# Kernel optimization log

Measured on AMD Instinct MI355X. Metric: run time of the kernel, lower is better.

## Reference

```python
import jax, jax.numpy as jnp
import numpy as np

D_MODEL = 1024
NUM_HEADS = 16
D_K = D_MODEL // NUM_HEADS


def setup_inputs() -> dict:
    key = jax.random.key(0)
    ks = jax.random.split(key, 7)
    B, S = 4, 2048
    scale = 1.0 / np.sqrt(D_MODEL)
    return {
        "query": jax.random.normal(ks[0], (B, S, D_MODEL), dtype=jnp.float32),
        "key": jax.random.normal(ks[1], (B, S, D_MODEL), dtype=jnp.float32),
        "value": jax.random.normal(ks[2], (B, S, D_MODEL), dtype=jnp.float32),
        "W_q": jax.random.normal(ks[3], (D_MODEL, D_MODEL), dtype=jnp.float32) * scale,
        "W_k": jax.random.normal(ks[4], (D_MODEL, D_MODEL), dtype=jnp.float32) * scale,
        "W_v": jax.random.normal(ks[5], (D_MODEL, D_MODEL), dtype=jnp.float32) * scale,
        "W_o": jax.random.normal(ks[6], (D_MODEL, D_MODEL), dtype=jnp.float32) * scale,
    }


def reference(query, key, value, W_q, W_k, W_v, W_o):
    B, S, _ = query.shape
    # nn.Linear applies x @ W.T; project then split heads: (B, H, S, d_k)
    def proj(x, W):
        return (x @ W.T).reshape(B, S, NUM_HEADS, D_K).transpose(0, 2, 1, 3)
    Q = proj(query, W_q)
    K = proj(key, W_k)
    V = proj(value, W_v)
    # naive full-score attention: (B, H, S, S)
    scores = jnp.einsum("bhqd,bhkd->bhqk", Q, K) / jnp.sqrt(jnp.float32(D_K))
    attn = jax.nn.softmax(scores, axis=-1)
    out = jnp.einsum("bhqk,bhkd->bhqd", attn, V)  # (B, H, S, d_k)
    out = out.transpose(0, 2, 1, 3).reshape(B, S, D_MODEL)
    return out @ W_o.T
```

## Files before the change

kernel.cpp:

```cpp
#include <hip/hip_runtime.h>
#include <hip/hip_bf16.h>
#include <cstdint>
#include <cstddef>

static constexpr int S  = 2048;
static constexpr int DM = 1024;
static constexpr int NH = 16;
static constexpr int BB = 4;
static constexpr int MR = BB * S;

typedef __bf16 bf16x8 __attribute__((ext_vector_type(8)));
typedef float  f32x4  __attribute__((ext_vector_type(4)));
typedef float  f32x16 __attribute__((ext_vector_type(16)));
typedef unsigned int uint2v __attribute__((ext_vector_type(2)));

__device__ __forceinline__ f32x4 mfma16(bf16x8 a, bf16x8 b, f32x4 c) {
    return __builtin_amdgcn_mfma_f32_16x16x32_bf16(a, b, c, 0, 0, 0);
}
__device__ __forceinline__ f32x16 mfma32(bf16x8 a, bf16x8 b, f32x16 c) {
    return __builtin_amdgcn_mfma_f32_32x32x16_bf16(a, b, c, 0, 0, 0);
}

__device__ __forceinline__ unsigned int cvt_pk_bf16(float lo, float hi) {
    unsigned int r;
    asm("v_cvt_pk_bf16_f32 %0, %1, %2" : "=v"(r) : "v"(lo), "v"(hi));
    return r;
}

struct CvtArgs {
    const float* src[7];
    __hip_bfloat16* dst[7];
    int n[7];
    float scl[7];
};

__global__ __launch_bounds__(256) void cvt_kernel(CvtArgs a) {
    const int t = blockIdx.y;
    const int i = (blockIdx.x * 256 + threadIdx.x) * 4;
    if (i >= a.n[t]) return;
    const float s = a.scl[t];
    const float4 v = *reinterpret_cast<const float4*>(a.src[t] + i);
    union { __hip_bfloat16 h[4]; short4 s4; } u;
    u.h[0] = __float2bfloat16(v.x * s);
    u.h[1] = __float2bfloat16(v.y * s);
    u.h[2] = __float2bfloat16(v.z * s);
    u.h[3] = __float2bfloat16(v.w * s);
    *reinterpret_cast<short4*>(a.dst[t] + i) = u.s4;
}

template<int SPLIT>
__global__ __launch_bounds__(256) void gemm_bt(
    const __hip_bfloat16* __restrict__ X,
    const __hip_bfloat16* __restrict__ W,
    void* __restrict__ Cout, int M, int N, int K)
{
    __shared__ __align__(16) unsigned char smem[65536];
    __hip_bfloat16* Ts = reinterpret_cast<__hip_bfloat16*>(smem);

    const int tid  = threadIdx.x;
    const int wave = tid >> 6, lane = tid & 63;
    const int wm = wave >> 1, wn = wave & 1;
    const int lr = lane & 15, lg = lane >> 4;
    const int m0 = blockIdx.y * 128;
    const int n0 = blockIdx.x * 128;

    const int srow = tid >> 3, scol = (tid & 7) * 8;

    auto stage = [&](int bsel, int kt) {
        __hip_bfloat16* As = reinterpret_cast<__hip_bfloat16*>(smem + bsel * 32768);
        __hip_bfloat16* Bs = reinterpret_cast<__hip_bfloat16*>(smem + bsel * 32768 + 16384);
#pragma unroll
        for (int r = 0; r < 4; ++r) {
            const int c = r * 256 + tid;
            const int row = srow + r * 32;
            __builtin_amdgcn_global_load_lds(
                (const __attribute__((address_space(1))) void*)&X[(size_t)(m0 + row) * K + kt + scol],
                (__attribute__((address_space(3))) void*)&As[c * 8], 16, 0, 0);
            __builtin_amdgcn_global_load_lds(
                (const __attribute__((address_space(1))) void*)&W[(size_t)(n0 + row) * K + kt + scol],
                (__attribute__((address_space(3))) void*)&Bs[c * 8], 16, 0, 0);
        }
    };

    f32x4 acc[4][4] = {};

    stage(0, 0);
    int cur = 0;
    for (int kt = 0; kt < K; kt += 64) {
        __syncthreads();
        if (kt + 64 < K) stage(cur ^ 1, kt + 64);

        const __hip_bfloat16* As = reinterpret_cast<const __hip_bfloat16*>(smem + cur * 32768);
        const __hip_bfloat16* Bs = reinterpret_cast<const __hip_bfloat16*>(smem + cur * 32768 + 16384);
#pragma unroll
        for (int ks = 0; ks < 2; ++ks) {
            bf16x8 af[4], bfr[4];
#pragma unroll
            for (int i = 0; i < 4; ++i)
                af[i] = *reinterpret_cast<const bf16x8*>(&As[(wm * 64 + i * 16 + lr) * 64 + ks * 32 + lg * 8]);
#pragma unroll
            for (int i = 0; i < 4; ++i)
                bfr[i] = *reinterpret_cast<const bf16x8*>(&Bs[(wn * 64 + i * 16 + lr) * 64 + ks * 32 + lg * 8]);
#pragma unroll
            for (int mi = 0; mi < 4; ++mi)
#pragma unroll
                for (int ni = 0; ni < 4; ++ni)
                    acc[mi][ni] = mfma16(af[mi], bfr[ni], acc[mi][ni]);
        }
        cur ^= 1;
    }

    if constexpr (SPLIT == 2) {
        __syncthreads();
#pragma unroll
        for (int mi = 0; mi < 4; ++mi)
#pragma unroll
            for (int ni = 0; ni < 4; ++ni)
#pragma unroll
                for (int j = 0; j < 4; ++j) {
                    const int nl = wn * 64 + ni * 16 + lr;
                    const int ml = wm * 64 + mi * 16 + lg * 4 + j;
                    Ts[nl * 136 + ml] = __float2bfloat16(acc[mi][ni][j]);
                }
        __syncthreads();
        __hip_bfloat16* VT = reinterpret_cast<__hip_bfloat16*>(Cout);
        const int b = m0 >> 11, s0 = m0 & (S - 1);
#pragma unroll
        for (int r = 0; r < 8; ++r) {
            const int idx = r * 256 + tid;
            const int nl = idx >> 4, mc = idx & 15;
            const uint4 val = *reinterpret_cast<const uint4*>(&Ts[nl * 136 + mc * 8]);
            const int h = (n0 + nl) >> 6, d = (n0 + nl) & 63;
            *reinterpret_cast<uint4*>(
                &VT[(((size_t)b * NH + h) * 64 + d) * S + s0 + mc * 8]) = val;
        }
    } else {
#pragma unroll
        for (int mi = 0; mi < 4; ++mi)
#pragma unroll
            for (int ni = 0; ni < 4; ++ni)
#pragma unroll
                for (int j = 0; j < 4; ++j) {
                    const int m = m0 + wm * 64 + mi * 16 + lg * 4 + j;
                    const int n = n0 + wn * 64 + ni * 16 + lr;
                    const float v = acc[mi][ni][j];
                    if constexpr (SPLIT == 1) {
                        const int b = m >> 11, s = m & (S - 1);
                        const int h = n >> 6,  d = n & 63;
                        reinterpret_cast<__hip_bfloat16*>(Cout)[
                            ((((size_t)b * NH + h) * S + s) << 6) + d] = __float2bfloat16(v);
                    } else {
                        reinterpret_cast<float*>(Cout)[(size_t)m * N + n] = v;
                    }
                }
    }
}

__global__ __launch_bounds__(256) void attn_kernel(
    const __hip_bfloat16* __restrict__ Qp,
    const __hip_bfloat16* __restrict__ Kp,
    const __hip_bfloat16* __restrict__ VpT,
    __hip_bfloat16* __restrict__ Oc)
{
    constexpr int LP = 72;
    constexpr int NT = S / 64;
    __shared__ __hip_bfloat16 Ks[2][64][LP];
    __shared__ __hip_bfloat16 Vt[2][64][LP];

    const int tid  = threadIdx.x;
    const int wave = tid >> 6, lane = tid & 63;
    const int l31 = lane & 31, hi = lane >> 5;

    const int id  = blockIdx.x;
    const int xcd = id & 7, idx = id >> 3;
    const int bh   = xcd + 8 * (idx >> 4);
    const int qblk = idx & 15;

    const int b = bh >> 4, h = bh & (NH - 1);
    const int q0 = qblk * 128 + wave * 32;

    const __hip_bfloat16* Qh  = Qp  + (size_t)bh * S * 64;
    const __hip_bfloat16* Kh  = Kp  + (size_t)bh * S * 64;
    const __hip_bfloat16* VhT = VpT + (size_t)bh * S * 64;

    const int srow0 = tid >> 3,         scol = (tid & 7) * 8;
    const int srow1 = (256 + tid) >> 3;

    bf16x8 qf[4];
#pragma unroll
    for (int ds = 0; ds < 4; ++ds)
        qf[ds] = *reinterpret_cast<const bf16x8*>(
            &Qh[(size_t)(q0 + l31) * 64 + ds * 16 + hi * 8]);

    bf16x8 onesf;
#pragma unroll
    for (int i = 0; i < 8; ++i) onesf[i] = (__bf16)1.0f;

    f32x16 o[2] = {};
    f32x16 osum = {};
    const f32x16 zero16 = {};

    uint4 kreg0, kreg1, vreg0, vreg1;
    kreg0 = *reinterpret_cast<const uint4*>(&Kh[(size_t)srow0 * 64 + scol]);
    kreg1 = *reinterpret_cast<const uint4*>(&Kh[(size_t)srow1 * 64 + scol]);
    vreg0 = *reinterpret_cast<const uint4*>(&VhT[(size_t)srow0 * S + scol]);
    vreg1 = *reinterpret_cast<const uint4*>(&VhT[(size_t)srow1 * S + scol]);
    *reinterpret_cast<uint4*>(&Ks[0][srow0][scol]) = kreg0;
    *reinterpret_cast<uint4*>(&Ks[0][srow1][scol]) = kreg1;
    *reinterpret_cast<uint4*>(&Vt[0][srow0][scol]) = vreg0;
    *reinterpret_cast<uint4*>(&Vt[0][srow1][scol]) = vreg1;

    for (int t = 0; t < NT; ++t) {
        const int cur = t & 1;
        __syncthreads();

        if (t + 1 < NT) {
            const int kt = (t + 1) * 64;
            kreg0 = *reinterpret_cast<const uint4*>(&Kh[(size_t)(kt + srow0) * 64 + scol]);
            kreg1 = *reinterpret_cast<const uint4*>(&Kh[(size_t)(kt + srow1) * 64 + scol]);
            vreg0 = *reinterpret_cast<const uint4*>(&VhT[(size_t)srow0 * S + kt + scol]);
            vreg1 = *reinterpret_cast<const uint4*>(&VhT[(size_t)srow1 * S + kt + scol]);
        }

        f32x16 scf[2];
        __builtin_amdgcn_s_setprio(1);
        {
            bf16x8 kfr0 = *reinterpret_cast<const bf16x8*>(&Ks[cur][l31][hi * 8]);
            bf16x8 kfr1 = *reinterpret_cast<const bf16x8*>(&Ks[cur][32 + l31][hi * 8]);
            scf[0] = mfma32(kfr0, qf[0], zero16);
            scf[1] = mfma32(kfr1, qf[0], zero16);
        }
#pragma unroll
        for (int ds = 1; ds < 4; ++ds) {
            bf16x8 kfr0 = *reinterpret_cast<const bf16x8*>(&Ks[cur][l31][ds * 16 + hi * 8]);
            bf16x8 kfr1 = *reinterpret_cast<const bf16x8*>(&Ks[cur][32 + l31][ds * 16 + hi * 8]);
            scf[0] = mfma32(kfr0, qf[ds], scf[0]);
            scf[1] = mfma32(kfr1, qf[ds], scf[1]);
        }
        __builtin_amdgcn_s_setprio(0);

        unsigned int w[2][8];
#pragma unroll
        for (int kf = 0; kf < 2; ++kf)
#pragma unroll
            for (int t8 = 0; t8 < 8; ++t8)
                w[kf][t8] = cvt_pk_bf16(
                    __builtin_amdgcn_exp2f(scf[kf][2 * t8]),
                    __builtin_amdgcn_exp2f(scf[kf][2 * t8 + 1]));

        __builtin_amdgcn_s_setprio(1);
#pragma unroll
        for (int kb = 0; kb < 4; ++kb) {
            const int kf = kb >> 1, tb = (kb & 1) * 4;
            uint2v r02 = __builtin_amdgcn_permlane32_swap(w[kf][tb + 0], w[kf][tb + 2], false, false);
            uint2v r13 = __builtin_amdgcn_permlane32_swap(w[kf][tb + 1], w[kf][tb + 3], false, false);
            union { unsigned int u[4]; bf16x8 v; } pf;
            pf.u[0] = r02[0]; pf.u[1] = r13[0]; pf.u[2] = r02[1]; pf.u[3] = r13[1];
            bf16x8 vf0 = *reinterpret_cast<const bf16x8*>(&Vt[cur][l31][kb * 16 + hi * 8]);
            bf16x8 vf1 = *reinterpret_cast<const bf16x8*>(&Vt[cur][32 + l31][kb * 16 + hi * 8]);
            o[0] = mfma32(pf.v, vf0, o[0]);
            o[1] = mfma32(pf.v, vf1, o[1]);
            osum = mfma32(pf.v, onesf, osum);
        }
        __builtin_amdgcn_s_setprio(0);

        if (t + 1 < NT) {
            const int nxt = cur ^ 1;
            *reinterpret_cast<uint4*>(&Ks[nxt][srow0][scol]) = kreg0;
            *reinterpret_cast<uint4*>(&Ks[nxt][srow1][scol]) = kreg1;
            *reinterpret_cast<uint4*>(&Vt[nxt][srow0][scol]) = vreg0;
            *reinterpret_cast<uint4*>(&Vt[nxt][srow1][scol]) = vreg1;
        }
    }

    float inv[16];
#pragma unroll
    for (int r = 0; r < 16; ++r) inv[r] = 1.0f / osum[r];
#pragma unroll
    for (int df = 0; df < 2; ++df)
#pragma unroll
        for (int r = 0; r < 16; ++r) {
            const int qrow = (r & 3) + 8 * (r >> 2) + 4 * hi;
            const size_t row = (size_t)b * S + q0 + qrow;
            const int col = h * 64 + df * 32 + l31;
            Oc[row * DM + col] = __float2bfloat16(o[df][r] * inv[r]);
        }
}

extern "C" void kernel_launch(void* const* d_in, const int* in_sizes, int n_in,
                              void* d_out, int out_size, void* d_ws, size_t ws_size,
                              hipStream_t stream)
{
    const float* q  = (const float*)d_in[0];
    const float* k  = (const float*)d_in[1];
    const float* v  = (const float*)d_in[2];
    const float* wq = (const float*)d_in[3];
    const float* wk = (const float*)d_in[4];
    const float* wv = (const float*)d_in[5];
    const float* wo = (const float*)d_in[6];

    const size_t NE = (size_t)MR * DM;
    const size_t WE = (size_t)DM * DM;

    const size_t need = (7 * NE + 4 * WE) * sizeof(__hip_bfloat16);
    if (ws_size < need) return;

    __hip_bfloat16* p   = (__hip_bfloat16*)d_ws;
    __hip_bfloat16* qb  = p; p += NE;
    __hip_bfloat16* kb  = p; p += NE;
    __hip_bfloat16* vb  = p; p += NE;
    __hip_bfloat16* wqb = p; p += WE;
    __hip_bfloat16* wkb = p; p += WE;
    __hip_bfloat16* wvb = p; p += WE;
    __hip_bfloat16* wob = p; p += WE;
    __hip_bfloat16* Qp  = p; p += NE;
    __hip_bfloat16* Kp  = p; p += NE;
    __hip_bfloat16* VpT = p; p += NE;
    __hip_bfloat16* Oc  = p; p += NE;

    constexpr float SC = 0.18033688011112042f;

    CvtArgs ca;
    ca.src[0] = q;  ca.src[1] = k;  ca.src[2] = v;
    ca.src[3] = wq; ca.src[4] = wk; ca.src[5] = wv; ca.src[6] = wo;
    ca.dst[0] = qb;  ca.dst[1] = kb;  ca.dst[2] = vb;
    ca.dst[3] = wqb; ca.dst[4] = wkb; ca.dst[5] = wvb; ca.dst[6] = wob;
    for (int i = 0; i < 7; ++i) {
        ca.n[i] = (i < 3) ? (int)NE : (int)WE;
        ca.scl[i] = (i == 3) ? SC : 1.0f;
    }

    cvt_kernel<<<dim3((unsigned)(NE / 1024), 7), 256, 0, stream>>>(ca);

    dim3 gg(DM / 128, MR / 128);
    gemm_bt<1><<<gg, 256, 0, stream>>>(qb, wqb, Qp,  MR, DM, DM);
    gemm_bt<1><<<gg, 256, 0, stream>>>(kb, wkb, Kp,  MR, DM, DM);
    gemm_bt<2><<<gg, 256, 0, stream>>>(vb, wvb, VpT, MR, DM, DM);

    attn_kernel<<<dim3(1024), 256, 0, stream>>>(Qp, Kp, VpT, Oc);

    gemm_bt<0><<<gg, 256, 0, stream>>>(Oc, wob, d_out, MR, DM, DM);
}
```

Baseline: 227.9 us.

## Fuse fp32-to-bf16 activation conversion into projection GEMM A-tile loads

```diff
diff --git a/kernel.cpp b/kernel.cpp
--- a/kernel.cpp
+++ b/kernel.cpp
@@ -28,10 +28,10 @@
 }
 
 struct CvtArgs {
-    const float* src[7];
-    __hip_bfloat16* dst[7];
-    int n[7];
-    float scl[7];
+    const float* src[4];
+    __hip_bfloat16* dst[4];
+    int n[4];
+    float scl[4];
 };
 
 __global__ __launch_bounds__(256) void cvt_kernel(CvtArgs a) {
@@ -48,14 +48,16 @@
     *reinterpret_cast<short4*>(a.dst[t] + i) = u.s4;
 }
 
-template<int SPLIT>
+template<int SPLIT, int FPA>
 __global__ __launch_bounds__(256) void gemm_bt(
-    const __hip_bfloat16* __restrict__ X,
+    const void* __restrict__ Xv,
     const __hip_bfloat16* __restrict__ W,
     void* __restrict__ Cout, int M, int N, int K)
 {
     __shared__ __align__(16) unsigned char smem[65536];
     __hip_bfloat16* Ts = reinterpret_cast<__hip_bfloat16*>(smem);
+    const float* Xf = reinterpret_cast<const float*>(Xv);
+    const __hip_bfloat16* Xb = reinterpret_cast<const __hip_bfloat16*>(Xv);
 
     const int tid  = threadIdx.x;
     const int wave = tid >> 6, lane = tid & 63;
@@ -66,29 +68,58 @@
 
     const int srow = tid >> 3, scol = (tid & 7) * 8;
 
-    auto stage = [&](int bsel, int kt) {
+    float4 areg[8];
+
+    auto issue = [&](int bsel, int kt) {
         __hip_bfloat16* As = reinterpret_cast<__hip_bfloat16*>(smem + bsel * 32768);
         __hip_bfloat16* Bs = reinterpret_cast<__hip_bfloat16*>(smem + bsel * 32768 + 16384);
 #pragma unroll
         for (int r = 0; r < 4; ++r) {
             const int c = r * 256 + tid;
             const int row = srow + r * 32;
-            __builtin_amdgcn_global_load_lds(
-                (const __attribute__((address_space(1))) void*)&X[(size_t)(m0 + row) * K + kt + scol],
-                (__attribute__((address_space(3))) void*)&As[c * 8], 16, 0, 0);
+            if constexpr (FPA) {
+                const float* src = &Xf[(size_t)(m0 + row) * K + kt + scol];
+                areg[2 * r]     = *reinterpret_cast<const float4*>(src);
+                areg[2 * r + 1] = *reinterpret_cast<const float4*>(src + 4);
+            } else {
+                __builtin_amdgcn_global_load_lds(
+                    (const __attribute__((address_space(1))) void*)&Xb[(size_t)(m0 + row) * K + kt + scol],
+                    (__attribute__((address_space(3))) void*)&As[c * 8], 16, 0, 0);
+            }
             __builtin_amdgcn_global_load_lds(
                 (const __attribute__((address_space(1))) void*)&W[(size_t)(n0 + row) * K + kt + scol],
                 (__attribute__((address_space(3))) void*)&Bs[c * 8], 16, 0, 0);
         }
     };
+    auto writeA = [&](int bsel) {
+        if constexpr (FPA) {
+            __hip_bfloat16* As = reinterpret_cast<__hip_bfloat16*>(smem + bsel * 32768);
+#pragma unroll
+            for (int r = 0; r < 4; ++r) {
+                const int c = r * 256 + tid;
+                union { __hip_bfloat16 h[8]; uint4 u4; } pk;
+                pk.h[0] = __float2bfloat16(areg[2 * r].x);
+                pk.h[1] = __float2bfloat16(areg[2 * r].y);
+                pk.h[2] = __float2bfloat16(areg[2 * r].z);
+                pk.h[3] = __float2bfloat16(areg[2 * r].w);
+                pk.h[4] = __float2bfloat16(areg[2 * r + 1].x);
+                pk.h[5] = __float2bfloat16(areg[2 * r + 1].y);
+                pk.h[6] = __float2bfloat16(areg[2 * r + 1].z);
+                pk.h[7] = __float2bfloat16(areg[2 * r + 1].w);
+                *reinterpret_cast<uint4*>(&As[c * 8]) = pk.u4;
+            }
+        }
+    };
 
     f32x4 acc[4][4] = {};
 
-    stage(0, 0);
+    issue(0, 0);
+    writeA(0);
     int cur = 0;
     for (int kt = 0; kt < K; kt += 64) {
         __syncthreads();
-        if (kt + 64 < K) stage(cur ^ 1, kt + 64);
+        const bool more = (kt + 64 < K);
+        if (more) issue(cur ^ 1, kt + 64);
 
         const __hip_bfloat16* As = reinterpret_cast<const __hip_bfloat16*>(smem + cur * 32768);
         const __hip_bfloat16* Bs = reinterpret_cast<const __hip_bfloat16*>(smem + cur * 32768 + 16384);
@@ -107,6 +138,7 @@
                 for (int ni = 0; ni < 4; ++ni)
                     acc[mi][ni] = mfma16(af[mi], bfr[ni], acc[mi][ni]);
         }
+        if (more) writeA(cur ^ 1);
         cur ^= 1;
     }
 
@@ -302,13 +334,10 @@
     const size_t NE = (size_t)MR * DM;
     const size_t WE = (size_t)DM * DM;
 
-    const size_t need = (7 * NE + 4 * WE) * sizeof(__hip_bfloat16);
+    const size_t need = (4 * NE + 4 * WE) * sizeof(__hip_bfloat16);
     if (ws_size < need) return;
 
     __hip_bfloat16* p   = (__hip_bfloat16*)d_ws;
-    __hip_bfloat16* qb  = p; p += NE;
-    __hip_bfloat16* kb  = p; p += NE;
-    __hip_bfloat16* vb  = p; p += NE;
     __hip_bfloat16* wqb = p; p += WE;
     __hip_bfloat16* wkb = p; p += WE;
     __hip_bfloat16* wvb = p; p += WE;
@@ -321,23 +350,21 @@
     constexpr float SC = 0.18033688011112042f;
 
     CvtArgs ca;
-    ca.src[0] = q;  ca.src[1] = k;  ca.src[2] = v;
-    ca.src[3] = wq; ca.src[4] = wk; ca.src[5] = wv; ca.src[6] = wo;
-    ca.dst[0] = qb;  ca.dst[1] = kb;  ca.dst[2] = vb;
-    ca.dst[3] = wqb; ca.dst[4] = wkb; ca.dst[5] = wvb; ca.dst[6] = wob;
-    for (int i = 0; i < 7; ++i) {
-        ca.n[i] = (i < 3) ? (int)NE : (int)WE;
-        ca.scl[i] = (i == 3) ? SC : 1.0f;
+    ca.src[0] = wq; ca.src[1] = wk; ca.src[2] = wv; ca.src[3] = wo;
+    ca.dst[0] = wqb; ca.dst[1] = wkb; ca.dst[2] = wvb; ca.dst[3] = wob;
+    for (int i = 0; i < 4; ++i) {
+        ca.n[i] = (int)WE;
+        ca.scl[i] = (i == 0) ? SC : 1.0f;
     }
 
-    cvt_kernel<<<dim3((unsigned)(NE / 1024), 7), 256, 0, stream>>>(ca);
+    cvt_kernel<<<dim3((unsigned)(WE / 1024), 4), 256, 0, stream>>>(ca);
 
     dim3 gg(DM / 128, MR / 128);
-    gemm_bt<1><<<gg, 256, 0, stream>>>(qb, wqb, Qp,  MR, DM, DM);
-    gemm_bt<1><<<gg, 256, 0, stream>>>(kb, wkb, Kp,  MR, DM, DM);
-    gemm_bt<2><<<gg, 256, 0, stream>>>(vb, wvb, VpT, MR, DM, DM);
+    gemm_bt<1, 1><<<gg, 256, 0, stream>>>((const void*)q, wqb, Qp,  MR, DM, DM);
+    gemm_bt<1, 1><<<gg, 256, 0, stream>>>((const void*)k, wkb, Kp,  MR, DM, DM);
+    gemm_bt<2, 1><<<gg, 256, 0, stream>>>((const void*)v, wvb, VpT, MR, DM, DM);
 
     attn_kernel<<<dim3(1024), 256, 0, stream>>>(Qp, Kp, VpT, Oc);
 
-    gemm_bt<0><<<gg, 256, 0, stream>>>(Oc, wob, d_out, MR, DM, DM);
-}
+    gemm_bt<0, 0><<<gg, 256, 0, stream>>>((const void*)Oc, wob, d_out, MR, DM, DM);
+}
```

After: 267.9 us. 17.6% more time.
